# Performance work log

Measured on AMD Instinct MI355X. Metric: run time of the kernel, lower is better.

## Reference

```python
import jax, jax.numpy as jnp
import numpy as np

TOPK = 3
IOU_THRESHOLD = 0.5


def setup_inputs() -> dict:
    key = jax.random.key(0)
    k0, k1, k2, k3 = jax.random.split(key, 4)
    S, N, TGT_PER_VID = 256, 128, 4
    M = S * TGT_PER_VID          # 1024 target moments total
    P = N * N                    # 16384 valid proposals (mask2d all ones)
    start_offset = jax.random.normal(k0, (S, P), dtype=jnp.float32) * 0.1
    end_offset = jax.random.normal(k1, (S, P), dtype=jnp.float32) * 0.1
    # target moments: (start, end) in [0,1], start <= end
    tgt_moments = jnp.sort(jax.random.uniform(k2, (M, 2), dtype=jnp.float32), axis=1)
    num_targets = jnp.full((S,), TGT_PER_VID, dtype=jnp.int32)  # sums to M
    iou2ds = jax.random.uniform(k3, (M, N, N), dtype=jnp.float32)
    mask2d = jnp.ones((N, N), dtype=bool)
    return {
        "start_offset": start_offset,
        "end_offset": end_offset,
        "tgt_moments": tgt_moments,
        "num_targets": num_targets,
        "iou2ds": iou2ds,
        "mask2d": mask2d,
    }


def reference(start_offset, end_offset, tgt_moments, num_targets, iou2ds, mask2d):
    M, N, _ = iou2ds.shape
    S, P = start_offset.shape
    # map each of the M targets back to its source video (repeat_interleave)
    scatter_m2s = jnp.repeat(jnp.arange(S), num_targets, total_repeat_length=M)
    so = start_offset[scatter_m2s]  # [M, P]
    eo = end_offset[scatter_m2s]    # [M, P]
    # row-major nonzero positions of mask2d (== torch masked_select ordering)
    rows, cols = jnp.nonzero(mask2d, size=P)
    iou1ds = iou2ds[:, rows, cols]  # [M, P]
    # top-k scatter mask + IoU-threshold mask
    _, topk_idx = jax.lax.top_k(iou1ds, TOPK)  # [M, TOPK]
    target_mask = jnp.zeros((M, P), dtype=start_offset.dtype)
    target_mask = target_mask.at[jnp.arange(M)[:, None], topk_idx].set(1.0)
    target_mask = jnp.where(iou1ds > IOU_THRESHOLD, 1.0, target_mask)
    # scores2ds_to_moments: proposal (row, col) -> moment (row/N, (col+1)/N)
    starts = rows.astype(start_offset.dtype) / N                 # [P]
    ends = (cols.astype(start_offset.dtype) + 1.0) / N           # [P]
    start_offset_target = tgt_moments[:, 0:1] - starts[None, :]  # [M, P]
    end_offset_target = tgt_moments[:, 1:2] - ends[None, :]      # [M, P]
    loss = jnp.abs(so - start_offset_target) + jnp.abs(eo - end_offset_target)
    return (loss * target_mask).sum() / target_mask.sum()
```

## Files before the change

kernel.cpp:

```cpp
#include <hip/hip_runtime.h>
#include <math.h>

#define TOPK_N 3
#define IOU_THR 0.5f
#define MAXN_TAB 4096
#define NCNT 64

__device__ __forceinline__ bool better(float va, int ia, float vb, int ib) {
    return (va > vb) || (va == vb && ia < ib);
}

__global__ void prep_kernel(const int* __restrict__ num_targets,
                            const int* __restrict__ mask2d,
                            int* __restrict__ scatter,
                            int* __restrict__ counts,
                            int S, int M, int P) {
    const int bid = blockIdx.x;
    const int tid = threadIdx.x;

    if (bid < NCNT) {
        const int P4 = P >> 2;
        const int4* __restrict__ m4 = (const int4*)mask2d;
        int c = 0;
        for (int q = bid * 256 + tid; q < P4; q += NCNT * 256) {
            const int4 v = m4[q];
            c += (v.x != 0) + (v.y != 0) + (v.z != 0) + (v.w != 0);
        }
        if (bid == 0) {
            for (int j = (P4 << 2) + tid; j < P; j += 256)
                c += (mask2d[j] != 0);
        }
        __shared__ int red[256];
        red[tid] = c;
        __syncthreads();
        for (int st = 128; st > 0; st >>= 1) {
            if (tid < st) red[tid] += red[tid + st];
            __syncthreads();
        }
        if (tid == 0) counts[bid] = red[0];
    } else {
        __shared__ int cum[1025];
        __shared__ int scn[256];
        const int chunk = (S + 255) / 256;
        const int sbase = tid * chunk;
        int local[4];
        int csum = 0;
        for (int k = 0; k < chunk && k < 4; ++k) {
            int s = sbase + k;
            int v = (s < S) ? num_targets[s] : 0;
            csum += v;
            local[k] = csum;
        }
        scn[tid] = csum;
        __syncthreads();
        for (int d = 1; d < 256; d <<= 1) {
            int v = scn[tid];
            int add = (tid >= d) ? scn[tid - d] : 0;
            __syncthreads();
            scn[tid] = v + add;
            __syncthreads();
        }
        {
            int excl = scn[tid] - csum;
            for (int k = 0; k < chunk && k < 4; ++k) {
                int s = sbase + k;
                if (s < S) cum[s + 1] = excl + local[k];
            }
            if (tid == 0) cum[0] = 0;
        }
        __syncthreads();
        const int total = cum[S];
        for (int m = tid; m < M; m += 256) {
            int mm = m;
            if (mm >= total) mm = (total > 0) ? (total - 1) : 0;
            int lo = 0, hi = S - 1;
            while (lo < hi) {
                int mid = (lo + hi) >> 1;
                if (cum[mid + 1] <= mm) lo = mid + 1; else hi = mid;
            }
            scatter[m] = lo;
        }
    }
}

__global__ void build_kernel(const int* __restrict__ counts,
                             const int* __restrict__ mask2d,
                             int* __restrict__ rcidx,
                             float* __restrict__ starts,
                             float* __restrict__ ends,
                             int* __restrict__ flag,
                             int N, int P) {
    const int tid = threadIdx.x;
    __shared__ int scan[256];

    scan[tid] = (tid < NCNT) ? counts[tid] : 0;
    __syncthreads();
    for (int st = 128; st > 0; st >>= 1) {
        if (tid < st) scan[tid] += scan[tid + st];
        __syncthreads();
    }
    const int K_all = scan[0];
    const int f = (K_all == P && (P & 3) == 0 && N <= MAXN_TAB) ? 1 : 0;
    if (tid == 0) flag[0] = f;
    if (f) return;
    __syncthreads();

    const int per = (P + 255) / 256;
    const int base = tid * per;
    int cnt = 0;
    for (int k = 0; k < per; ++k) {
        int j = base + k;
        if (j < P && mask2d[j] != 0) cnt++;
    }
    scan[tid] = cnt;
    __syncthreads();
    for (int d = 1; d < 256; d <<= 1) {
        int v = scan[tid];
        int add = (tid >= d) ? scan[tid - d] : 0;
        __syncthreads();
        scan[tid] = v + add;
        __syncthreads();
    }
    const int K = scan[255];
    int pos = scan[tid] - cnt;

    const float fN = (float)N;
    for (int k = 0; k < per; ++k) {
        int j = base + k;
        if (j < P && mask2d[j] != 0) {
            int r = j / N;
            int c = j - r * N;
            rcidx[pos]  = j;
            starts[pos] = (float)r / fN;
            ends[pos]   = (float)(c + 1) / fN;
            pos++;
        }
    }
    __syncthreads();
    for (int j = K + tid; j < P; j += 256) {
        rcidx[j]  = 0;
        starts[j] = 0.0f;
        ends[j]   = 1.0f / fN;
    }
}

__global__ __launch_bounds__(256)
void loss_kernel(const float* __restrict__ start_offset,
                 const float* __restrict__ end_offset,
                 const float* __restrict__ tgt_moments,
                 const int* __restrict__ scatter,
                 const float* __restrict__ iou2ds,
                 const int* __restrict__ rcidx,
                 const float* __restrict__ starts,
                 const float* __restrict__ ends,
                 double* __restrict__ psum,
                 int* __restrict__ pcnt,
                 const int* __restrict__ flag,
                 int P, int M, int N) {
    const int bid = blockIdx.x;
    const int m = ((M & 7) == 0) ? ((bid & 7) * (M >> 3) + (bid >> 3)) : bid;
    const int tid = threadIdx.x;
    const int s   = scatter[m];
    const int fp  = flag[0];

    const float* __restrict__ so_row  = start_offset + (size_t)s * P;
    const float* __restrict__ eo_row  = end_offset   + (size_t)s * P;
    const float* __restrict__ iou_row = iou2ds       + (size_t)m * P;
    const float tgt0 = tgt_moments[2 * m];
    const float tgt1 = tgt_moments[2 * m + 1];

    extern __shared__ float tabs[];
    float* st_tab = tabs;
    float* en_tab = tabs + N;
    if (fp) {
        const float fN = (float)N;
        for (int i = tid; i < N; i += 256) {
            st_tab[i] = (float)i / fN;
            en_tab[i] = (float)(i + 1) / fN;
        }
        __syncthreads();
    }

    double lsum = 0.0;
    int    lcnt = 0;

    float v0 = -INFINITY, v1 = -INFINITY, v2 = -INFINITY;
    int   i0 = 0x7fffffff, i1 = 0x7fffffff, i2 = 0x7fffffff;

#define PROC(v, jj, so_, eo_, st_, en_)                                         \
    do {                                                                        \
        if (better(v, jj, v2, i2)) {                                            \
            if (better(v, jj, v1, i1)) {                                        \
                v2 = v1; i2 = i1;                                               \
                if (better(v, jj, v0, i0)) { v1 = v0; i1 = i0; v0 = v; i0 = jj; } \
                else                       { v1 = v;  i1 = jj; }                \
            } else { v2 = v; i2 = jj; }                                         \
        }                                                                       \
        if (v > IOU_THR) {                                                      \
            const float sot = tgt0 - (st_);                                     \
            const float eot = tgt1 - (en_);                                     \
            lsum += (double)(fabsf((so_) - sot) + fabsf((eo_) - eot));          \
            lcnt++;                                                             \
        }                                                                       \
    } while (0)

    if (fp) {
        const float4* __restrict__ iou4 = (const float4*)iou_row;
        const float4* __restrict__ so4  = (const float4*)so_row;
        const float4* __restrict__ eo4  = (const float4*)eo_row;
        const int P4 = P >> 2;
        for (int q = tid; q < P4; q += 256) {
            const float4 vi = iou4[q];
            const float4 vs = so4[q];
            const float4 ve = eo4[q];
            const int j = q << 2;
            int r = j / N;
            int c = j - r * N;
            PROC(vi.x, j + 0, vs.x, ve.x, st_tab[r], en_tab[c]);
            c++; if (c == N) { c = 0; r++; }
            PROC(vi.y, j + 1, vs.y, ve.y, st_tab[r], en_tab[c]);
            c++; if (c == N) { c = 0; r++; }
            PROC(vi.z, j + 2, vs.z, ve.z, st_tab[r], en_tab[c]);
            c++; if (c == N) { c = 0; r++; }
            PROC(vi.w, j + 3, vs.w, ve.w, st_tab[r], en_tab[c]);
        }
    } else {
        for (int j = tid; j < P; j += 256) {
            const int   idx = rcidx[j];
            const float v   = iou_row[idx];
            PROC(v, j, so_row[j], eo_row[j], starts[j], ends[j]);
        }
    }
#undef PROC

    __shared__ float sv[256][3];
    __shared__ int   si[256][3];
    sv[tid][0] = v0; sv[tid][1] = v1; sv[tid][2] = v2;
    si[tid][0] = i0; si[tid][1] = i1; si[tid][2] = i2;
    __syncthreads();

    for (int str = 128; str > 0; str >>= 1) {
        if (tid < str) {
            float av0 = sv[tid][0], av1 = sv[tid][1], av2 = sv[tid][2];
            int   ai0 = si[tid][0], ai1 = si[tid][1], ai2 = si[tid][2];
            float bv0 = sv[tid + str][0], bv1 = sv[tid + str][1], bv2 = sv[tid + str][2];
            int   bi0 = si[tid + str][0], bi1 = si[tid + str][1], bi2 = si[tid + str][2];

            bool t0 = better(av0, ai0, bv0, bi0);
            float ov0 = t0 ? av0 : bv0;  int oi0 = t0 ? ai0 : bi0;
            float ahv = t0 ? av1 : av0;  int ahi = t0 ? ai1 : ai0;
            float a2v = t0 ? av2 : av1;  int a2i = t0 ? ai2 : ai1;
            float bhv = t0 ? bv0 : bv1;  int bhi = t0 ? bi0 : bi1;
            float b2v = t0 ? bv1 : bv2;  int b2i = t0 ? bi1 : bi2;

            bool t1 = better(ahv, ahi, bhv, bhi);
            float ov1 = t1 ? ahv : bhv;  int oi1 = t1 ? ahi : bhi;
            float cav = t1 ? a2v : ahv;  int cai = t1 ? a2i : ahi;
            float cbv = t1 ? bhv : b2v;  int cbi = t1 ? bhi : b2i;

            bool t2 = better(cav, cai, cbv, cbi);
            float ov2 = t2 ? cav : cbv;  int oi2 = t2 ? cai : cbi;

            sv[tid][0] = ov0; sv[tid][1] = ov1; sv[tid][2] = ov2;
            si[tid][0] = oi0; si[tid][1] = oi1; si[tid][2] = oi2;
        }
        __syncthreads();
    }

    if (tid < TOPK_N) {
        const float v = sv[0][tid];
        const int   j = si[0][tid];
        if (j != 0x7fffffff && !(v > IOU_THR)) {
            float stj, enj;
            if (fp) {
                int r = j / N, c = j - r * N;
                stj = st_tab[r]; enj = en_tab[c];
            } else {
                stj = starts[j]; enj = ends[j];
            }
            const float sot = tgt0 - stj;
            const float eot = tgt1 - enj;
            lsum += (double)(fabsf(so_row[j] - sot) + fabsf(eo_row[j] - eot));
            lcnt++;
        }
    }

    __shared__ double dsum[256];
    __shared__ int    dcnt[256];
    dsum[tid] = lsum; dcnt[tid] = lcnt;
    __syncthreads();
    for (int str = 128; str > 0; str >>= 1) {
        if (tid < str) { dsum[tid] += dsum[tid + str]; dcnt[tid] += dcnt[tid + str]; }
        __syncthreads();
    }
    if (tid == 0) {
        psum[bid] = dsum[0];
        pcnt[bid] = dcnt[0];
    }
}

__global__ void finalize_kernel(const double* __restrict__ psum,
                                const int* __restrict__ pcnt,
                                int M, float* __restrict__ out) {
    __shared__ double sd[256];
    __shared__ int    sc[256];
    const int tid = threadIdx.x;
    double a = 0.0;
    int    c = 0;
    for (int i = tid; i < M; i += 256) { a += psum[i]; c += pcnt[i]; }
    sd[tid] = a; sc[tid] = c;
    __syncthreads();
    for (int str = 128; str > 0; str >>= 1) {
        if (tid < str) { sd[tid] += sd[tid + str]; sc[tid] += sc[tid + str]; }
        __syncthreads();
    }
    if (tid == 0) out[0] = (float)(sd[0] / (double)sc[0]);
}

extern "C" void kernel_launch(void* const* d_in, const int* in_sizes, int n_in,
                              void* d_out, int out_size, void* d_ws, size_t ws_size,
                              hipStream_t stream) {
    const float* start_offset = (const float*)d_in[0];
    const float* end_offset   = (const float*)d_in[1];
    const float* tgt_moments  = (const float*)d_in[2];
    const int*   num_targets  = (const int*)d_in[3];
    const float* iou2ds       = (const float*)d_in[4];
    const int*   mask2d       = (const int*)d_in[5];

    const int S = in_sizes[3];
    const int M = in_sizes[2] / 2;
    const int P = in_sizes[0] / S;
    const int NN = in_sizes[5];
    int N = 1;
    while ((long long)N * N < (long long)NN) N++;

    char* ws = (char*)d_ws;
    size_t off = 0;
    int*    flag    = (int*)(ws + off);    off += 16;
    int*    counts  = (int*)(ws + off);    off += (NCNT * 4 + 15) & ~(size_t)15;
    int*    scatter = (int*)(ws + off);    off += ((size_t)M * 4 + 15) & ~(size_t)15;
    int*    rcidx   = (int*)(ws + off);    off += ((size_t)P * 4 + 15) & ~(size_t)15;
    float*  starts  = (float*)(ws + off);  off += ((size_t)P * 4 + 15) & ~(size_t)15;
    float*  ends    = (float*)(ws + off);  off += ((size_t)P * 4 + 15) & ~(size_t)15;
    double* psum    = (double*)(ws + off); off += ((size_t)M * 8 + 15) & ~(size_t)15;
    int*    pcnt    = (int*)(ws + off);    off += ((size_t)M * 4 + 15) & ~(size_t)15;

    const size_t tab_bytes = (size_t)2 * N * sizeof(float);

    prep_kernel<<<NCNT + 1, 256, 0, stream>>>(num_targets, mask2d, scatter, counts,
                                              S, M, P);
    build_kernel<<<1, 256, 0, stream>>>(counts, mask2d, rcidx, starts, ends, flag, N, P);
    loss_kernel<<<M, 256, tab_bytes, stream>>>(start_offset, end_offset, tgt_moments,
                                               scatter, iou2ds, rcidx, starts, ends,
                                               psum, pcnt, flag, P, M, N);
    finalize_kernel<<<1, 256, 0, stream>>>(psum, pcnt, M, (float*)d_out);
}
```

Measured before the change: 42.77 us.

## Use 512-thread blocks, branchless top-k, shuffle reductions, and computed moment coordinates

Raises the loss kernel to 512 threads per block and replaces the shared-memory start/end tables with shift/mask index math plus multiplication by 1/N. The fast path now requires N to be a power of two. The per-element top-3 insertion becomes branchless selects, and the partial loss sum accumulates in float instead of double. The shared-memory tree reductions are replaced by wavefront shuffle reductions followed by a single-thread merge across waves, which removes many barriers. Risks are some precision change from float accumulation and the top-k tie-breaking now relying on strict '>' within each thread.

```diff
diff --git a/kernel.cpp b/kernel.cpp
--- a/kernel.cpp
+++ b/kernel.cpp
@@ -3,11 +3,32 @@
 
 #define TOPK_N 3
 #define IOU_THR 0.5f
-#define MAXN_TAB 4096
 #define NCNT 64
+#define THREADS 512
+#define NW (THREADS / 64)
+#define SENT 0x7fffffff
 
 __device__ __forceinline__ bool better(float va, int ia, float vb, int ib) {
     return (va > vb) || (va == vb && ia < ib);
+}
+
+__device__ __forceinline__ void merge3(float& a0, float& a1, float& a2,
+                                       int& x0, int& x1, int& x2,
+                                       float b0, float b1, float b2,
+                                       int y0, int y1, int y2) {
+    bool t0 = better(a0, x0, b0, y0);
+    float ov0 = t0 ? a0 : b0;  int oi0 = t0 ? x0 : y0;
+    float ahv = t0 ? a1 : a0;  int ahi = t0 ? x1 : x0;
+    float a2v = t0 ? a2 : a1;  int a2i = t0 ? x2 : x1;
+    float bhv = t0 ? b0 : b1;  int bhi = t0 ? y0 : y1;
+    float b2v = t0 ? b1 : b2;  int b2i = t0 ? y1 : y2;
+    bool t1 = better(ahv, ahi, bhv, bhi);
+    float ov1 = t1 ? ahv : bhv; int oi1 = t1 ? ahi : bhi;
+    float cav = t1 ? a2v : ahv; int cai = t1 ? a2i : ahi;
+    float cbv = t1 ? bhv : b2v; int cbi = t1 ? bhi : b2i;
+    bool t2 = better(cav, cai, cbv, cbi);
+    a0 = ov0; a1 = ov1; a2 = t2 ? cav : cbv;
+    x0 = oi0; x1 = oi1; x2 = t2 ? cai : cbi;
 }
 
 __global__ void prep_kernel(const int* __restrict__ num_targets,
@@ -100,7 +121,7 @@
         __syncthreads();
     }
     const int K_all = scan[0];
-    const int f = (K_all == P && (P & 3) == 0 && N <= MAXN_TAB) ? 1 : 0;
+    const int f = (K_all == P && (P & 3) == 0 && (N & (N - 1)) == 0) ? 1 : 0;
     if (tid == 0) flag[0] = f;
     if (f) return;
     __syncthreads();
@@ -144,7 +165,7 @@
     }
 }
 
-__global__ __launch_bounds__(256)
+__global__ __launch_bounds__(THREADS, 8)
 void loss_kernel(const float* __restrict__ start_offset,
                  const float* __restrict__ end_offset,
                  const float* __restrict__ tgt_moments,
@@ -169,39 +190,28 @@
     const float tgt0 = tgt_moments[2 * m];
     const float tgt1 = tgt_moments[2 * m + 1];
 
-    extern __shared__ float tabs[];
-    float* st_tab = tabs;
-    float* en_tab = tabs + N;
-    if (fp) {
-        const float fN = (float)N;
-        for (int i = tid; i < N; i += 256) {
-            st_tab[i] = (float)i / fN;
-            en_tab[i] = (float)(i + 1) / fN;
-        }
-        __syncthreads();
-    }
-
-    double lsum = 0.0;
-    int    lcnt = 0;
+    const int   lgN  = 31 - __clz(N);
+    const float invN = 1.0f / (float)N;
+
+    float lsum = 0.0f;
+    int   lcnt = 0;
 
     float v0 = -INFINITY, v1 = -INFINITY, v2 = -INFINITY;
-    int   i0 = 0x7fffffff, i1 = 0x7fffffff, i2 = 0x7fffffff;
-
-#define PROC(v, jj, so_, eo_, st_, en_)                                         \
-    do {                                                                        \
-        if (better(v, jj, v2, i2)) {                                            \
-            if (better(v, jj, v1, i1)) {                                        \
-                v2 = v1; i2 = i1;                                               \
-                if (better(v, jj, v0, i0)) { v1 = v0; i1 = i0; v0 = v; i0 = jj; } \
-                else                       { v1 = v;  i1 = jj; }                \
-            } else { v2 = v; i2 = jj; }                                         \
-        }                                                                       \
-        if (v > IOU_THR) {                                                      \
-            const float sot = tgt0 - (st_);                                     \
-            const float eot = tgt1 - (en_);                                     \
-            lsum += (double)(fabsf((so_) - sot) + fabsf((eo_) - eot));          \
-            lcnt++;                                                             \
-        }                                                                       \
+    int   i0 = SENT, i1 = SENT, i2 = SENT;
+
+#define PROC(v, jj, so_, eo_, st_, en_)                                     \
+    do {                                                                    \
+        const bool b0 = (v) > v0;                                           \
+        const bool b1 = (v) > v1;                                           \
+        const bool b2 = (v) > v2;                                           \
+        v2 = b1 ? v1 : (b2 ? (v) : v2);  i2 = b1 ? i1 : (b2 ? (jj) : i2);   \
+        v1 = b0 ? v0 : (b1 ? (v) : v1);  i1 = b0 ? i0 : (b1 ? (jj) : i1);   \
+        v0 = b0 ? (v) : v0;              i0 = b0 ? (jj) : i0;               \
+        const bool sel = (v) > IOU_THR;                                     \
+        const float l_ = fabsf((so_) - (tgt0 - (st_))) +                    \
+                         fabsf((eo_) - (tgt1 - (en_)));                     \
+        lsum += sel ? l_ : 0.0f;                                            \
+        lcnt += sel ? 1 : 0;                                                \
     } while (0)
 
     if (fp) {
@@ -209,23 +219,25 @@
         const float4* __restrict__ so4  = (const float4*)so_row;
         const float4* __restrict__ eo4  = (const float4*)eo_row;
         const int P4 = P >> 2;
-        for (int q = tid; q < P4; q += 256) {
+        for (int q = tid; q < P4; q += THREADS) {
             const float4 vi = iou4[q];
             const float4 vs = so4[q];
             const float4 ve = eo4[q];
-            const int j = q << 2;
-            int r = j / N;
-            int c = j - r * N;
-            PROC(vi.x, j + 0, vs.x, ve.x, st_tab[r], en_tab[c]);
-            c++; if (c == N) { c = 0; r++; }
-            PROC(vi.y, j + 1, vs.y, ve.y, st_tab[r], en_tab[c]);
-            c++; if (c == N) { c = 0; r++; }
-            PROC(vi.z, j + 2, vs.z, ve.z, st_tab[r], en_tab[c]);
-            c++; if (c == N) { c = 0; r++; }
-            PROC(vi.w, j + 3, vs.w, ve.w, st_tab[r], en_tab[c]);
+            const int j  = q << 2;
+            const int r  = j >> lgN;
+            const int c0 = j & (N - 1);
+            const float st = (float)r * invN;
+            const float e0 = (float)(c0 + 1) * invN;
+            const float e1 = (float)(c0 + 2) * invN;
+            const float e2 = (float)(c0 + 3) * invN;
+            const float e3 = (float)(c0 + 4) * invN;
+            PROC(vi.x, j + 0, vs.x, ve.x, st, e0);
+            PROC(vi.y, j + 1, vs.y, ve.y, st, e1);
+            PROC(vi.z, j + 2, vs.z, ve.z, st, e2);
+            PROC(vi.w, j + 3, vs.w, ve.w, st, e3);
         }
     } else {
-        for (int j = tid; j < P; j += 256) {
+        for (int j = tid; j < P; j += THREADS) {
             const int   idx = rcidx[j];
             const float v   = iou_row[idx];
             PROC(v, j, so_row[j], eo_row[j], starts[j], ends[j]);
@@ -233,69 +245,59 @@
     }
 #undef PROC
 
-    __shared__ float sv[256][3];
-    __shared__ int   si[256][3];
-    sv[tid][0] = v0; sv[tid][1] = v1; sv[tid][2] = v2;
-    si[tid][0] = i0; si[tid][1] = i1; si[tid][2] = i2;
-    __syncthreads();
-
-    for (int str = 128; str > 0; str >>= 1) {
-        if (tid < str) {
-            float av0 = sv[tid][0], av1 = sv[tid][1], av2 = sv[tid][2];
-            int   ai0 = si[tid][0], ai1 = si[tid][1], ai2 = si[tid][2];
-            float bv0 = sv[tid + str][0], bv1 = sv[tid + str][1], bv2 = sv[tid + str][2];
-            int   bi0 = si[tid + str][0], bi1 = si[tid + str][1], bi2 = si[tid + str][2];
-
-            bool t0 = better(av0, ai0, bv0, bi0);
-            float ov0 = t0 ? av0 : bv0;  int oi0 = t0 ? ai0 : bi0;
-            float ahv = t0 ? av1 : av0;  int ahi = t0 ? ai1 : ai0;
-            float a2v = t0 ? av2 : av1;  int a2i = t0 ? ai2 : ai1;
-            float bhv = t0 ? bv0 : bv1;  int bhi = t0 ? bi0 : bi1;
-            float b2v = t0 ? bv1 : bv2;  int b2i = t0 ? bi1 : bi2;
-
-            bool t1 = better(ahv, ahi, bhv, bhi);
-            float ov1 = t1 ? ahv : bhv;  int oi1 = t1 ? ahi : bhi;
-            float cav = t1 ? a2v : ahv;  int cai = t1 ? a2i : ahi;
-            float cbv = t1 ? bhv : b2v;  int cbi = t1 ? bhi : b2i;
-
-            bool t2 = better(cav, cai, cbv, cbi);
-            float ov2 = t2 ? cav : cbv;  int oi2 = t2 ? cai : cbi;
-
-            sv[tid][0] = ov0; sv[tid][1] = ov1; sv[tid][2] = ov2;
-            si[tid][0] = oi0; si[tid][1] = oi1; si[tid][2] = oi2;
-        }
-        __syncthreads();
-    }
-
-    if (tid < TOPK_N) {
-        const float v = sv[0][tid];
-        const int   j = si[0][tid];
-        if (j != 0x7fffffff && !(v > IOU_THR)) {
-            float stj, enj;
-            if (fp) {
-                int r = j / N, c = j - r * N;
-                stj = st_tab[r]; enj = en_tab[c];
-            } else {
-                stj = starts[j]; enj = ends[j];
-            }
-            const float sot = tgt0 - stj;
-            const float eot = tgt1 - enj;
-            lsum += (double)(fabsf(so_row[j] - sot) + fabsf(eo_row[j] - eot));
-            lcnt++;
-        }
-    }
-
-    __shared__ double dsum[256];
-    __shared__ int    dcnt[256];
-    dsum[tid] = lsum; dcnt[tid] = lcnt;
-    __syncthreads();
-    for (int str = 128; str > 0; str >>= 1) {
-        if (tid < str) { dsum[tid] += dsum[tid + str]; dcnt[tid] += dcnt[tid + str]; }
-        __syncthreads();
-    }
+    for (int d = 1; d < 64; d <<= 1) {
+        float bv0 = __shfl_xor(v0, d), bv1 = __shfl_xor(v1, d), bv2 = __shfl_xor(v2, d);
+        int   by0 = __shfl_xor(i0, d), by1 = __shfl_xor(i1, d), by2 = __shfl_xor(i2, d);
+        merge3(v0, v1, v2, i0, i1, i2, bv0, bv1, bv2, by0, by1, by2);
+    }
+    double dsum = (double)lsum;
+    for (int d = 1; d < 64; d <<= 1) dsum += __shfl_xor(dsum, d);
+    for (int d = 1; d < 64; d <<= 1) lcnt += __shfl_xor(lcnt, d);
+
+    __shared__ float  wv[NW][3];
+    __shared__ int    wi[NW][3];
+    __shared__ double wsum[NW];
+    __shared__ int    wcnt[NW];
+    const int wid  = tid >> 6;
+    const int lane = tid & 63;
+    if (lane == 0) {
+        wv[wid][0] = v0; wv[wid][1] = v1; wv[wid][2] = v2;
+        wi[wid][0] = i0; wi[wid][1] = i1; wi[wid][2] = i2;
+        wsum[wid] = dsum; wcnt[wid] = lcnt;
+    }
+    __syncthreads();
+
     if (tid == 0) {
-        psum[bid] = dsum[0];
-        pcnt[bid] = dcnt[0];
+        float a0 = wv[0][0], a1 = wv[0][1], a2 = wv[0][2];
+        int   x0 = wi[0][0], x1 = wi[0][1], x2 = wi[0][2];
+        double S = wsum[0];
+        int    C = wcnt[0];
+        for (int w = 1; w < NW; ++w) {
+            merge3(a0, a1, a2, x0, x1, x2,
+                   wv[w][0], wv[w][1], wv[w][2],
+                   wi[w][0], wi[w][1], wi[w][2]);
+            S += wsum[w];
+            C += wcnt[w];
+        }
+#define ADDTOP(vk, jk)                                                      \
+        do {                                                                \
+            if ((jk) != SENT && !((vk) > IOU_THR)) {                        \
+                float st_, en_;                                             \
+                if (fp) {                                                   \
+                    int r_ = (jk) >> lgN, c_ = (jk) & (N - 1);              \
+                    st_ = (float)r_ * invN; en_ = (float)(c_ + 1) * invN;   \
+                } else { st_ = starts[jk]; en_ = ends[jk]; }                \
+                S += (double)(fabsf(so_row[jk] - (tgt0 - st_)) +            \
+                              fabsf(eo_row[jk] - (tgt1 - en_)));            \
+                C += 1;                                                     \
+            }                                                               \
+        } while (0)
+        ADDTOP(a0, x0);
+        ADDTOP(a1, x1);
+        ADDTOP(a2, x2);
+#undef ADDTOP
+        psum[bid] = S;
+        pcnt[bid] = C;
     }
 }
 
@@ -345,13 +347,11 @@
     double* psum    = (double*)(ws + off); off += ((size_t)M * 8 + 15) & ~(size_t)15;
     int*    pcnt    = (int*)(ws + off);    off += ((size_t)M * 4 + 15) & ~(size_t)15;
 
-    const size_t tab_bytes = (size_t)2 * N * sizeof(float);
-
     prep_kernel<<<NCNT + 1, 256, 0, stream>>>(num_targets, mask2d, scatter, counts,
                                               S, M, P);
     build_kernel<<<1, 256, 0, stream>>>(counts, mask2d, rcidx, starts, ends, flag, N, P);
-    loss_kernel<<<M, 256, tab_bytes, stream>>>(start_offset, end_offset, tgt_moments,
-                                               scatter, iou2ds, rcidx, starts, ends,
-                                               psum, pcnt, flag, P, M, N);
+    loss_kernel<<<M, THREADS, 0, stream>>>(start_offset, end_offset, tgt_moments,
+                                           scatter, iou2ds, rcidx, starts, ends,
+                                           psum, pcnt, flag, P, M, N);
     finalize_kernel<<<1, 256, 0, stream>>>(psum, pcnt, M, (float*)d_out);
 }
```

After: 36.26 us. -15.2%, faster.
